# Kernel tuning notes

Hardware: AMD Instinct MI355X
Metric: run time of the kernel (lower is better)

## Reference

```python
import jax, jax.numpy as jnp
import numpy as np

# Model dims (match init_kwargs)
D_MODEL = 2048
H = 16        # query heads
HKV = 4       # kv heads (GQA)
DS = 32       # semantic head dim (compressed)
DG = 32       # geometric head dim (compressed, RoPE'd)
DV = 64       # value head dim
B, T = 2, 4096
MB = 64       # mem_block
LW = 1024     # local_window
ROPE_BASE = 10000.0
NEG_INF = -1e9


def _rope(x, pos, base):
    # x: [B, h, T, d] with d even; standard rotate-half RoPE
    d = x.shape[-1]
    inv_freq = 1.0 / (base ** (jnp.arange(0, d, 2, dtype=jnp.float32) / d))
    ang = pos.astype(jnp.float32)[:, None] * inv_freq          # [T, d/2]
    cos, sin = jnp.cos(ang), jnp.sin(ang)                      # [T, d/2]
    x1, x2 = jnp.split(x, 2, axis=-1)
    return jnp.concatenate([x1 * cos - x2 * sin,
                            x2 * cos + x1 * sin], axis=-1)


def setup_inputs() -> dict:
    key = jax.random.key(0)
    ks = jax.random.split(key, 8)
    w = lambda k, sh: jax.random.normal(k, sh, jnp.float32) * 0.02
    return {
        "x": jax.random.normal(ks[0], (B, T, D_MODEL), jnp.float32),
        "Wq_sem": w(ks[1], (D_MODEL, H * DS)),
        "Wk_sem": w(ks[2], (D_MODEL, HKV * DS)),
        "Wq_geo": w(ks[3], (D_MODEL, H * DG)),
        "Wk_geo": w(ks[4], (D_MODEL, HKV * DG)),
        "Wv": w(ks[5], (D_MODEL, HKV * DV)),
        "Wo": w(ks[6], (H * DV, D_MODEL)),
        "logit_scale": jnp.zeros((H,), jnp.float32),
    }


def reference(x, Wq_sem, Wk_sem, Wq_geo, Wk_geo, Wv, Wo, logit_scale):
    Bq, Tq = x.shape[0], x.shape[1]
    split = lambda y, h, d: y.reshape(Bq, Tq, h, d).transpose(0, 2, 1, 3)
    # Decoupled projections
    q_sem = split(x @ Wq_sem, H, DS)      # [B,H,T,DS]
    k_sem = split(x @ Wk_sem, HKV, DS)    # [B,HKV,T,DS]
    q_geo = split(x @ Wq_geo, H, DG)
    k_geo = split(x @ Wk_geo, HKV, DG)
    v = split(x @ Wv, HKV, DV)            # [B,HKV,T,DV]
    pos = jnp.arange(Tq)
    # RoPE only on the geometric path
    q_geo = _rope(q_geo, pos, ROPE_BASE)
    k_geo = _rope(k_geo, pos, ROPE_BASE)
    # Memory-block summarization: mean-pool remote KV into one token per block
    remote = Tq - LW
    nblk = remote // MB
    pool = lambda a: jnp.concatenate(
        [a[:, :, :remote].reshape(Bq, HKV, nblk, MB, a.shape[-1]).mean(axis=3),
         a[:, :, remote:]], axis=2)
    k_sem2, k_geo2, v2 = pool(k_sem), pool(k_geo), pool(v)  # [B,HKV,K,*], K=nblk+LW
    k_pos = jnp.concatenate([jnp.arange(nblk) * MB + (MB - 1),
                             jnp.arange(remote, Tq)])        # [K]
    # GQA head-group broadcast
    rep = lambda a: jnp.repeat(a, H // HKV, axis=1)
    k_sem2, k_geo2, v2 = rep(k_sem2), rep(k_geo2), rep(v2)   # [B,H,K,*]
    # Decoupled scores: semantic + geometric, each with its own scale
    scores = (jnp.einsum('bhqd,bhkd->bhqk', q_sem, k_sem2) * (1.0 / jnp.sqrt(float(DS)))
              + jnp.einsum('bhqd,bhkd->bhqk', q_geo, k_geo2) * (1.0 / jnp.sqrt(float(DG))))
    # Learned per-head temperature
    scores = scores * jnp.exp(logit_scale)[None, :, None, None]
    # Causal mask over summarized key positions
    mask = k_pos[None, :] <= pos[:, None]                    # [T,K]
    scores = jnp.where(mask[None, None], scores, NEG_INF)
    probs = jax.nn.softmax(scores, axis=-1)
    out = jnp.einsum('bhqk,bhkd->bhqd', probs, v2)           # [B,H,T,DV]
    out = out.transpose(0, 2, 1, 3).reshape(Bq, Tq, H * DV)
    return out @ Wo                                          # [B,T,D_MODEL]
```

## Files before the change

### kernel.cpp

```cpp
#include <hip/hip_runtime.h>
#include <math.h>

#define B_  2
#define T_  4096
#define DM  2048
#define H_  16
#define HKV 4
#define DV_ 64
#define MB_ 64
#define LW_ 1024
#define REMOTE 3072
#define NBLK 48
#define KTOT 1072
#define NTILES 17

typedef __bf16 bf16x8 __attribute__((ext_vector_type(8)));
typedef float  f32x4  __attribute__((ext_vector_type(4)));

__device__ __forceinline__ float bf2f(unsigned short u) {
    unsigned int x = ((unsigned int)u) << 16;
    return __builtin_bit_cast(float, x);
}
__device__ __forceinline__ unsigned short f2bf(float f) {
    unsigned int x = __builtin_bit_cast(unsigned int, f);
    x = x + 0x7fffu + ((x >> 16) & 1u);
    return (unsigned short)(x >> 16);
}

__device__ __forceinline__ void gload16(const unsigned short* gsrc,
                                        unsigned short* ldst) {
    __builtin_amdgcn_global_load_lds(
        (const __attribute__((address_space(1))) void*)gsrc,
        (__attribute__((address_space(3))) void*)ldst,
        16, 0, 0);
}

__global__ void cvt_f32_to_bf16(const float* __restrict__ src,
                                unsigned short* __restrict__ dst, int n) {
    int i = (blockIdx.x * blockDim.x + threadIdx.x) * 4;
    if (i >= n) return;
    float4 v = *(const float4*)(src + i);
    ushort4 o;
    o.x = f2bf(v.x); o.y = f2bf(v.y); o.z = f2bf(v.z); o.w = f2bf(v.w);
    *(ushort4*)(dst + i) = o;
}

__global__ void transpose_cvt(const float* __restrict__ src,
                              unsigned short* __restrict__ dst, int R, int C) {
    __shared__ float tile[32][33];
    int ct = blockIdx.x, rt = blockIdx.y;
    int tx = threadIdx.x, ty = threadIdx.y;
    #pragma unroll
    for (int i = ty; i < 32; i += 8)
        tile[i][tx] = src[(size_t)(rt * 32 + i) * C + ct * 32 + tx];
    __syncthreads();
    #pragma unroll
    for (int i = ty; i < 32; i += 8)
        dst[(size_t)(ct * 32 + i) * R + rt * 32 + tx] = f2bf(tile[tx][i]);
}

template<int MODE>
__global__ __launch_bounds__(512, 2) void gemm8p(
    const unsigned short* __restrict__ A,
    const unsigned short* __restrict__ BT,
    float* __restrict__ outF,
    unsigned short* __restrict__ qcat,
    unsigned short* __restrict__ kp,
    unsigned short* __restrict__ vt,
    int M, int N, int K, int nbx)
{
    extern __shared__ __align__(16) unsigned short lds[];

    const int tid = threadIdx.x;
    const int lane = tid & 63, w = tid >> 6;
    const int wm = w >> 2, wn = w & 3;
    const int l15 = lane & 15, lg = lane >> 4;

    const int cpx = gridDim.x >> 3;
    const int swz = (blockIdx.x & 7) * cpx + (blockIdx.x >> 3);
    const int bx = swz % nbx, by = swz / nbx;
    const int row0 = by * 256, col0 = bx * 256;

    const unsigned short* Ag = A  + (size_t)row0 * K;
    const unsigned short* Bg = BT + (size_t)col0 * K;

    const int sr0 = w * 16 + (lane >> 2);
    const int sr1 = sr0 + 128;
    const int sc0 = ((lane & 3) ^ ((sr0 >> 1) & 3)) << 3;

    const int rdsw = (lg ^ ((l15 >> 1) & 3)) << 3;
    const int aoff = (wm * 128 + l15) * 32 + rdsw;
    const int boff = (wn * 64 + l15) * 32 + rdsw;

    const int NT = K >> 5;
    f32x4 acc[8][4] = {};

    auto stageA = [&](int slot, int kk) {
        unsigned short* sa = lds + slot * 16384;
        gload16(Ag + (size_t)sr0 * K + kk + sc0, sa + w * 512);
        gload16(Ag + (size_t)sr1 * K + kk + sc0, sa + 4096 + w * 512);
    };
    auto stageB = [&](int slot, int kk) {
        unsigned short* sb = lds + slot * 16384 + 8192;
        gload16(Bg + (size_t)sr0 * K + kk + sc0, sb + w * 512);
        gload16(Bg + (size_t)sr1 * K + kk + sc0, sb + 4096 + w * 512);
    };

    stageA(0, 0);  stageB(0, 0);
    stageA(1, 32); stageB(1, 32);
    stageA(2, 64); stageB(2, 64);
    asm volatile("s_waitcnt vmcnt(8)" ::: "memory");

    for (int t = 0; t < NT; ++t) {
        __builtin_amdgcn_s_barrier();
        const unsigned short* As_ = lds + (t & 3) * 16384;
        const unsigned short* Bs_ = As_ + 8192;
        const int wslot = (t + 3) & 3;
        const int kk3 = (t + 3) << 5;
        const bool st = (t + 3) < NT;

        if (st) stageA(wslot, kk3);
        bf16x8 bfr[4], af[4];
        #pragma unroll
        for (int nf = 0; nf < 4; nf++)
            bfr[nf] = __builtin_bit_cast(bf16x8, *(const uint4*)&Bs_[boff + nf * 512]);
        #pragma unroll
        for (int mf = 0; mf < 4; mf++)
            af[mf] = __builtin_bit_cast(bf16x8, *(const uint4*)&As_[aoff + mf * 512]);
        __builtin_amdgcn_s_setprio(1);
        #pragma unroll
        for (int mf = 0; mf < 4; mf++)
            #pragma unroll
            for (int nf = 0; nf < 4; nf++)
                acc[mf][nf] = __builtin_amdgcn_mfma_f32_16x16x32_bf16(
                                  af[mf], bfr[nf], acc[mf][nf], 0, 0, 0);
        __builtin_amdgcn_s_setprio(0);

        if (st) stageB(wslot, kk3);
        bf16x8 af2[4];
        #pragma unroll
        for (int mf = 0; mf < 4; mf++)
            af2[mf] = __builtin_bit_cast(bf16x8, *(const uint4*)&As_[aoff + (mf + 4) * 512]);
        __builtin_amdgcn_s_setprio(1);
        #pragma unroll
        for (int mf = 0; mf < 4; mf++)
            #pragma unroll
            for (int nf = 0; nf < 4; nf++)
                acc[mf + 4][nf] = __builtin_amdgcn_mfma_f32_16x16x32_bf16(
                                      af2[mf], bfr[nf], acc[mf + 4][nf], 0, 0, 0);
        __builtin_amdgcn_s_setprio(0);

        if (t + 3 < NT)      asm volatile("s_waitcnt vmcnt(8)" ::: "memory");
        else if (t + 2 < NT) asm volatile("s_waitcnt vmcnt(4)" ::: "memory");
        else if (t + 1 < NT) asm volatile("s_waitcnt vmcnt(0)" ::: "memory");
    }

    const int rbase = wm * 128;
    if (MODE == 1) {
        #pragma unroll
        for (int mf = 0; mf < 8; mf++)
            #pragma unroll
            for (int nf = 0; nf < 4; nf++)
                #pragma unroll
                for (int r = 0; r < 4; r++) {
                    int row = row0 + rbase + mf * 16 + lg * 4 + r;
                    int col = col0 + wn * 64 + nf * 16 + l15;
                    outF[(size_t)row * N + col] = acc[mf][nf][r];
                }
    } else {
        const int cspan = col0 + wn * 64;
        const int tbase = row0 & 4095;
        const int bq = row0 >> 12;

        if ((cspan >= 512 && cspan < 1024) || (cspan >= 1152 && cspan < 1280)) {
            const float invf = exp2f(-(float)l15 * 0.8304820237218406f);
            #pragma unroll
            for (int mf = 0; mf < 8; mf++) {
                #pragma unroll
                for (int r = 0; r < 4; r++) {
                    float s, c;
                    sincosf((float)(tbase + rbase + mf*16 + lg*4 + r) * invf, &s, &c);
                    float a0 = acc[mf][0][r], a1 = acc[mf][1][r];
                    acc[mf][0][r] = a0 * c - a1 * s;
                    acc[mf][1][r] = a1 * c + a0 * s;
                    float a2 = acc[mf][2][r], a3 = acc[mf][3][r];
                    acc[mf][2][r] = a2 * c - a3 * s;
                    acc[mf][3][r] = a3 * c + a2 * s;
                }
            }
        }

        if (cspan < 1024) {
            #pragma unroll
            for (int nf = 0; nf < 4; nf++) {
                int col = cspan + nf * 16 + l15;
                int h = (col < 512) ? (col >> 5) : ((col - 512) >> 5);
                int d = (col < 512) ? (col & 31) : (32 + (col & 31));
                unsigned short* qb =
                    qcat + (((size_t)(bq * 16 + h)) * 4096 + tbase) * 64 + d;
                #pragma unroll
                for (int mf = 0; mf < 8; mf++)
                    #pragma unroll
                    for (int r = 0; r < 4; r++)
                        qb[(size_t)(rbase + mf*16 + lg*4 + r) * 64] =
                            f2bf(acc[mf][nf][r]);
            }
        } else if (tbase >= REMOTE) {
            #pragma unroll
            for (int nf = 0; nf < 4; nf++) {
                int col = cspan + nf * 16 + l15;
                #pragma unroll
                for (int mf = 0; mf < 8; mf++)
                    #pragma unroll
                    for (int r = 0; r < 4; r++) {
                        int key = tbase + rbase + mf*16 + lg*4 + r - 3024;
                        unsigned short hv = f2bf(acc[mf][nf][r]);
                        if (col < 1280) {
                            int g, dk;
                            if (col < 1152) { g = (col - 1024) >> 5; dk = col & 31; }
                            else            { g = (col - 1152) >> 5; dk = 32 + (col & 31); }
                            kp[(((size_t)(bq*4 + g)) * KTOT + key) * 64 + dk] = hv;
                        } else {
                            int g = (col - 1280) >> 6, dv = col & 63;
                            vt[(((size_t)(bq*4 + g)) * 64 + dv) * KTOT + key] = hv;
                        }
                    }
            }
        } else {
            #pragma unroll
            for (int half = 0; half < 2; half++) {
                #pragma unroll
                for (int nf = 0; nf < 4; nf++) {
                    float ps = 0.f;
                    #pragma unroll
                    for (int mf = half * 4; mf < half * 4 + 4; mf++)
                        #pragma unroll
                        for (int r = 0; r < 4; r++) ps += acc[mf][nf][r];
                    ps += __shfl_xor(ps, 16);
                    ps += __shfl_xor(ps, 32);
                    if (lane < 16) {
                        int col = cspan + nf * 16 + l15;
                        int key = ((tbase + rbase) >> 6) + half;
                        unsigned short hv = f2bf(ps * (1.f / 64.f));
                        if (col < 1280) {
                            int g, dk;
                            if (col < 1152) { g = (col - 1024) >> 5; dk = col & 31; }
                            else            { g = (col - 1152) >> 5; dk = 32 + (col & 31); }
                            kp[(((size_t)(bq*4 + g)) * KTOT + key) * 64 + dk] = hv;
                        } else {
                            int g = (col - 1280) >> 6, dv = col & 63;
                            vt[(((size_t)(bq*4 + g)) * 64 + dv) * KTOT + key] = hv;
                        }
                    }
                }
            }
        }
    }
}

__global__ __launch_bounds__(256) void attn_fwd(
    const unsigned short* __restrict__ qcat,
    const unsigned short* __restrict__ kp,
    const unsigned short* __restrict__ vt,
    const float* __restrict__ ls,
    unsigned short* __restrict__ attn_out)
{
    __shared__ unsigned short Pl[4][32][72];

    const int tid = threadIdx.x;
    const int lane = tid & 63, w = tid >> 6;
    const int l15 = lane & 15, lg = lane >> 4;

    const int wid = blockIdx.x * 4 + w;
    const int hb = wid & 31;
    const int iu = wid >> 5;
    int i;
    if (iu < 32)       i = 127 - iu;
    else if (iu == 32) i = 0;
    else if (iu == 33) i = 1;
    else               i = iu - 32;
    const int h = hb & 15, b = hb >> 4, g = h >> 2;
    const int q0 = i * 32;

    int ktmax;
    if (q0 < 64) ktmax = NTILES;
    else {
        int lastkey = q0 + 31 - 3024;
        ktmax = (lastkey < NBLK) ? 1 : (lastkey / 64 + 1);
    }

    const float sc = __expf(ls[h]) * 0.17677669529663687f;

    bf16x8 aq[2][2];
    const unsigned short* qbase = qcat + (((size_t)(b * 16 + h)) * T_ + q0) * 64;
    #pragma unroll
    for (int rf = 0; rf < 2; rf++)
        #pragma unroll
        for (int kh = 0; kh < 2; kh++)
            aq[rf][kh] = __builtin_bit_cast(bf16x8,
                *(const uint4*)(qbase + (size_t)(rf*16 + l15)*64 + kh*32 + lg*8));

    float m[2][4], lrun[2][4];
    #pragma unroll
    for (int rf = 0; rf < 2; rf++)
        #pragma unroll
        for (int r = 0; r < 4; r++) { m[rf][r] = -1e9f; lrun[rf][r] = 0.f; }
    f32x4 oacc[2][4] = {};

    const unsigned short* kbase = kp + ((size_t)(b * 4 + g)) * KTOT * 64;
    const unsigned short* vbase = vt + ((size_t)(b * 4 + g)) * 64 * KTOT;

    for (int kt = 0; kt < ktmax; kt++) {
        const int kb = kt * 64;

        bf16x8 bk[4][2];
        #pragma unroll
        for (int nf = 0; nf < 4; nf++) {
            int krow = kb + nf*16 + l15;
            int krc = krow < KTOT ? krow : KTOT - 1;
            #pragma unroll
            for (int kh = 0; kh < 2; kh++)
                bk[nf][kh] = __builtin_bit_cast(bf16x8,
                    *(const uint4*)(kbase + (size_t)krc * 64 + kh*32 + lg*8));
        }

        f32x4 s[2][4] = {};
        #pragma unroll
        for (int rf = 0; rf < 2; rf++)
            #pragma unroll
            for (int nf = 0; nf < 4; nf++)
                #pragma unroll
                for (int kh = 0; kh < 2; kh++)
                    s[rf][nf] = __builtin_amdgcn_mfma_f32_16x16x32_bf16(
                                    aq[rf][kh], bk[nf][kh], s[rf][nf], 0, 0, 0);

        bf16x8 bv[4][2];
        #pragma unroll
        for (int nfv = 0; nfv < 4; nfv++)
            #pragma unroll
            for (int kh = 0; kh < 2; kh++) {
                int kc = kb + kh*32 + lg*8;
                int kcc = (kc + 8 <= KTOT) ? kc : KTOT - 8;
                bv[nfv][kh] = __builtin_bit_cast(bf16x8,
                    *(const uint4*)(vbase + (size_t)(nfv*16 + l15) * KTOT + kcc));
            }

        #pragma unroll
        for (int rf = 0; rf < 2; rf++) {
            #pragma unroll
            for (int r = 0; r < 4; r++) {
                const int qpos = q0 + rf*16 + lg*4 + r;
                float vals[4];
                float tmax = -INFINITY;
                #pragma unroll
                for (int nf = 0; nf < 4; nf++) {
                    int key = kb + nf*16 + l15;
                    float v = s[rf][nf][r] * sc;
                    int kpos = (key < NBLK) ? key * 64 + 63 : 3024 + key;
                    v = (key < KTOT) ? ((kpos <= qpos) ? v : -1e9f) : -INFINITY;
                    vals[nf] = v;
                    tmax = fmaxf(tmax, v);
                }
                #pragma unroll
                for (int d = 1; d < 16; d <<= 1)
                    tmax = fmaxf(tmax, __shfl_xor(tmax, d));
                float mn = fmaxf(m[rf][r], tmax);
                float scl = __expf(m[rf][r] - mn);
                m[rf][r] = mn;
                float rs = 0.f;
                #pragma unroll
                for (int nf = 0; nf < 4; nf++) {
                    unsigned short pb = f2bf(__expf(vals[nf] - mn));
                    rs += bf2f(pb);
                    Pl[w][rf*16 + lg*4 + r][nf*16 + l15] = pb;
                }
                #pragma unroll
                for (int d = 1; d < 16; d <<= 1)
                    rs += __shfl_xor(rs, d);
                lrun[rf][r] = lrun[rf][r] * scl + rs;
                #pragma unroll
                for (int nfv = 0; nfv < 4; nfv++)
                    oacc[rf][nfv][r] *= scl;
            }
        }

        #pragma unroll
        for (int rf = 0; rf < 2; rf++) {
            bf16x8 pa[2];
            #pragma unroll
            for (int kh = 0; kh < 2; kh++)
                pa[kh] = __builtin_bit_cast(bf16x8,
                    *(const uint4*)&Pl[w][rf*16 + l15][kh*32 + lg*8]);
            #pragma unroll
            for (int nfv = 0; nfv < 4; nfv++)
                #pragma unroll
                for (int kh = 0; kh < 2; kh++)
                    oacc[rf][nfv] = __builtin_amdgcn_mfma_f32_16x16x32_bf16(
                                        pa[kh], bv[nfv][kh], oacc[rf][nfv], 0, 0, 0);
        }
    }

    #pragma unroll
    for (int rf = 0; rf < 2; rf++) {
        #pragma unroll
        for (int r = 0; r < 4; r++) {
            float inv = 1.f / lrun[rf][r];
            int q = q0 + rf*16 + lg*4 + r;
            size_t obase = ((size_t)(b * T_ + q)) * 1024 + h * 64;
            #pragma unroll
            for (int nfv = 0; nfv < 4; nfv++)
                attn_out[obase + nfv*16 + l15] = f2bf(oacc[rf][nfv][r] * inv);
        }
    }
}

extern "C" void kernel_launch(void* const* d_in, const int* in_sizes, int n_in,
                              void* d_out, int out_size, void* d_ws, size_t ws_size,
                              hipStream_t stream) {
    const float* x      = (const float*)d_in[0];
    const float* Wq_sem = (const float*)d_in[1];
    const float* Wk_sem = (const float*)d_in[2];
    const float* Wq_geo = (const float*)d_in[3];
    const float* Wk_geo = (const float*)d_in[4];
    const float* Wv     = (const float*)d_in[5];
    const float* Wo     = (const float*)d_in[6];
    const float* ls     = (const float*)d_in[7];

    char* w = (char*)d_ws;
    auto alloc = [&](size_t bytes) {
        char* p = w;
        w += (bytes + 255) & ~(size_t)255;
        return p;
    };
    unsigned short* xb    = (unsigned short*)alloc((size_t)8192 * 2048 * 2);
    unsigned short* WcatT = (unsigned short*)alloc((size_t)1536 * 2048 * 2);
    unsigned short* WoT   = (unsigned short*)alloc((size_t)2048 * 1024 * 2);
    unsigned short* qcat  = (unsigned short*)alloc((size_t)2 * 16 * 4096 * 64 * 2);
    unsigned short* kp    = (unsigned short*)alloc((size_t)2 * 4 * 1072 * 64 * 2);
    unsigned short* vt    = (unsigned short*)alloc((size_t)2 * 4 * 1072 * 64 * 2);
    unsigned short* aout  = (unsigned short*)alloc((size_t)8192 * 1024 * 2);

    hipFuncSetAttribute(reinterpret_cast<const void*>(&gemm8p<0>),
                        hipFuncAttributeMaxDynamicSharedMemorySize, 131072);
    hipFuncSetAttribute(reinterpret_cast<const void*>(&gemm8p<1>),
                        hipFuncAttributeMaxDynamicSharedMemorySize, 131072);

    cvt_f32_to_bf16<<<16384, 256, 0, stream>>>(x, xb, 8192 * 2048);

    dim3 tb(32, 8);
    transpose_cvt<<<dim3(16, 64), tb, 0, stream>>>(Wq_sem, WcatT + (size_t)0    * 2048, 2048, 512);
    transpose_cvt<<<dim3(16, 64), tb, 0, stream>>>(Wq_geo, WcatT + (size_t)512  * 2048, 2048, 512);
    transpose_cvt<<<dim3( 4, 64), tb, 0, stream>>>(Wk_sem, WcatT + (size_t)1024 * 2048, 2048, 128);
    transpose_cvt<<<dim3( 4, 64), tb, 0, stream>>>(Wk_geo, WcatT + (size_t)1152 * 2048, 2048, 128);
    transpose_cvt<<<dim3( 8, 64), tb, 0, stream>>>(Wv,     WcatT + (size_t)1280 * 2048, 2048, 256);
    transpose_cvt<<<dim3(64, 32), tb, 0, stream>>>(Wo, WoT, 1024, 2048);

    gemm8p<0><<<192, 512, 131072, stream>>>(
        xb, WcatT, nullptr, qcat, kp, vt, 8192, 1536, 2048, 6);

    attn_fwd<<<dim3(1024), 256, 0, stream>>>(qcat, kp, vt, ls, aout);

    gemm8p<1><<<256, 512, 131072, stream>>>(
        aout, WoT, (float*)d_out, nullptr, nullptr, nullptr, 8192, 2048, 1024, 8);
}
```

Measured before the change: 214.4 us.

## Restructure GEMM main loop into K=64 ping-pong with fine-grained staged loads

Rewrites the bf16 GEMM mainloop so that each LDS stage covers a K=64 slice (two MFMA k-steps), double-buffered as A0/B0 and A1/B1. Each stage is split into four sub-phases over quadrants of the 8x4 accumulator tile, and the global-to-LDS loads for the next tile are interleaved between them under barriers, using a new 8-way XOR swizzle. The aim is better overlap of global loads with MFMA work and fewer LDS reads per MFMA, at the cost of many more barriers per iteration.

```diff
diff --git a/kernel.cpp b/kernel.cpp
--- a/kernel.cpp
+++ b/kernel.cpp
@@ -60,7 +60,7 @@
 }
 
 template<int MODE>
-__global__ __launch_bounds__(512, 2) void gemm8p(
+__global__ __launch_bounds__(512, 2) void gemm8f(
     const unsigned short* __restrict__ A,
     const unsigned short* __restrict__ BT,
     float* __restrict__ outF,
@@ -84,76 +84,209 @@
     const unsigned short* Ag = A  + (size_t)row0 * K;
     const unsigned short* Bg = BT + (size_t)col0 * K;
 
-    const int sr0 = w * 16 + (lane >> 2);
-    const int sr1 = sr0 + 128;
-    const int sc0 = ((lane & 3) ^ ((sr0 >> 1) & 3)) << 3;
-
-    const int rdsw = (lg ^ ((l15 >> 1) & 3)) << 3;
-    const int aoff = (wm * 128 + l15) * 32 + rdsw;
-    const int boff = (wn * 64 + l15) * 32 + rdsw;
-
-    const int NT = K >> 5;
+    unsigned short* const A0 = lds;
+    unsigned short* const B0 = lds + 16384;
+    unsigned short* const A1 = lds + 32768;
+    unsigned short* const B1 = lds + 49152;
+
+    const int srow  = w * 8 + (lane >> 3);
+    const int scol8 = ((lane & 7) ^ ((lane >> 3) & 7)) * 8;
+
+    const int l7 = lane & 7;
+    const int p0 = ((lg) ^ l7) * 8;
+    const int p1 = ((4 + lg) ^ l7) * 8;
+    const int arow = (wm * 128 + l15) * 64;
+    const int brow = (wn * 64 + l15) * 64;
+
+    const int NT = K >> 6;
+    const int NI = NT >> 1;
     f32x4 acc[8][4] = {};
 
-    auto stageA = [&](int slot, int kk) {
-        unsigned short* sa = lds + slot * 16384;
-        gload16(Ag + (size_t)sr0 * K + kk + sc0, sa + w * 512);
-        gload16(Ag + (size_t)sr1 * K + kk + sc0, sa + 4096 + w * 512);
+    auto stgA = [&](unsigned short* Ab, int half, int tt) {
+        unsigned short* hb = Ab + half * 8192;
+        const unsigned short* src =
+            Ag + (size_t)(half * 128 + srow) * K + tt * 64 + scol8;
+        gload16(src, hb + w * 512);
+        gload16(src + (size_t)64 * K, hb + 4096 + w * 512);
     };
-    auto stageB = [&](int slot, int kk) {
-        unsigned short* sb = lds + slot * 16384 + 8192;
-        gload16(Bg + (size_t)sr0 * K + kk + sc0, sb + w * 512);
-        gload16(Bg + (size_t)sr1 * K + kk + sc0, sb + 4096 + w * 512);
+    auto stgB = [&](unsigned short* Bb, int half, int tt) {
+        unsigned short* hb = Bb + half * 8192;
+        const unsigned short* src =
+            Bg + (size_t)(half * 128 + srow) * K + tt * 64 + scol8;
+        gload16(src, hb + w * 512);
+        gload16(src + (size_t)64 * K, hb + 4096 + w * 512);
     };
 
-    stageA(0, 0);  stageB(0, 0);
-    stageA(1, 32); stageB(1, 32);
-    stageA(2, 64); stageB(2, 64);
-    asm volatile("s_waitcnt vmcnt(8)" ::: "memory");
-
-    for (int t = 0; t < NT; ++t) {
-        __builtin_amdgcn_s_barrier();
-        const unsigned short* As_ = lds + (t & 3) * 16384;
-        const unsigned short* Bs_ = As_ + 8192;
-        const int wslot = (t + 3) & 3;
-        const int kk3 = (t + 3) << 5;
-        const bool st = (t + 3) < NT;
-
-        if (st) stageA(wslot, kk3);
-        bf16x8 bfr[4], af[4];
-        #pragma unroll
-        for (int nf = 0; nf < 4; nf++)
-            bfr[nf] = __builtin_bit_cast(bf16x8, *(const uint4*)&Bs_[boff + nf * 512]);
-        #pragma unroll
-        for (int mf = 0; mf < 4; mf++)
-            af[mf] = __builtin_bit_cast(bf16x8, *(const uint4*)&As_[aoff + mf * 512]);
-        __builtin_amdgcn_s_setprio(1);
-        #pragma unroll
-        for (int mf = 0; mf < 4; mf++)
-            #pragma unroll
-            for (int nf = 0; nf < 4; nf++)
-                acc[mf][nf] = __builtin_amdgcn_mfma_f32_16x16x32_bf16(
-                                  af[mf], bfr[nf], acc[mf][nf], 0, 0, 0);
-        __builtin_amdgcn_s_setprio(0);
-
-        if (st) stageB(wslot, kk3);
-        bf16x8 af2[4];
-        #pragma unroll
-        for (int mf = 0; mf < 4; mf++)
-            af2[mf] = __builtin_bit_cast(bf16x8, *(const uint4*)&As_[aoff + (mf + 4) * 512]);
-        __builtin_amdgcn_s_setprio(1);
-        #pragma unroll
-        for (int mf = 0; mf < 4; mf++)
-            #pragma unroll
-            for (int nf = 0; nf < 4; nf++)
-                acc[mf + 4][nf] = __builtin_amdgcn_mfma_f32_16x16x32_bf16(
-                                      af2[mf], bfr[nf], acc[mf + 4][nf], 0, 0, 0);
-        __builtin_amdgcn_s_setprio(0);
-
-        if (t + 3 < NT)      asm volatile("s_waitcnt vmcnt(8)" ::: "memory");
-        else if (t + 2 < NT) asm volatile("s_waitcnt vmcnt(4)" ::: "memory");
-        else if (t + 1 < NT) asm volatile("s_waitcnt vmcnt(0)" ::: "memory");
+    #define LDF(base, off) __builtin_bit_cast(bf16x8, *(const uint4*)&(base)[off])
+
+    stgB(B0, 0, 0); stgB(B0, 1, 0);
+    stgA(A0, 0, 0); stgA(A0, 1, 0);
+    stgB(B1, 0, 1); stgB(B1, 1, 1);
+    asm volatile("s_waitcnt vmcnt(4)" ::: "memory");
+    __builtin_amdgcn_s_barrier();
+
+    for (int i = 0; i < NI; ++i) {
+        const int t0 = 2 * i;
+        const bool st2 = (t0 + 2) < NT;
+        bf16x8 af[4][2], b01[2][2], b23[2][2];
+
+        #pragma unroll
+        for (int mf = 0; mf < 4; mf++) {
+            af[mf][0] = LDF(A0, arow + mf * 1024 + p0);
+            af[mf][1] = LDF(A0, arow + mf * 1024 + p1);
+        }
+        #pragma unroll
+        for (int nf = 0; nf < 2; nf++) {
+            b01[nf][0] = LDF(B0, brow + nf * 1024 + p0);
+            b01[nf][1] = LDF(B0, brow + nf * 1024 + p1);
+        }
+        stgA(A1, 0, t0 + 1);
+        __builtin_amdgcn_s_barrier();
+        __builtin_amdgcn_s_setprio(1);
+        #pragma unroll
+        for (int mf = 0; mf < 4; mf++)
+            #pragma unroll
+            for (int nf = 0; nf < 2; nf++)
+                #pragma unroll
+                for (int ks = 0; ks < 2; ks++)
+                    acc[mf][nf] = __builtin_amdgcn_mfma_f32_16x16x32_bf16(
+                        af[mf][ks], b01[nf][ks], acc[mf][nf], 0, 0, 0);
+        __builtin_amdgcn_s_setprio(0);
+        __builtin_amdgcn_s_barrier();
+
+        #pragma unroll
+        for (int nf = 0; nf < 2; nf++) {
+            b23[nf][0] = LDF(B0, brow + (nf + 2) * 1024 + p0);
+            b23[nf][1] = LDF(B0, brow + (nf + 2) * 1024 + p1);
+        }
+        stgA(A1, 1, t0 + 1);
+        __builtin_amdgcn_s_barrier();
+        __builtin_amdgcn_s_setprio(1);
+        #pragma unroll
+        for (int mf = 0; mf < 4; mf++)
+            #pragma unroll
+            for (int nf = 0; nf < 2; nf++)
+                #pragma unroll
+                for (int ks = 0; ks < 2; ks++)
+                    acc[mf][nf + 2] = __builtin_amdgcn_mfma_f32_16x16x32_bf16(
+                        af[mf][ks], b23[nf][ks], acc[mf][nf + 2], 0, 0, 0);
+        __builtin_amdgcn_s_setprio(0);
+        __builtin_amdgcn_s_barrier();
+
+        #pragma unroll
+        for (int mf = 0; mf < 4; mf++) {
+            af[mf][0] = LDF(A0, arow + (mf + 4) * 1024 + p0);
+            af[mf][1] = LDF(A0, arow + (mf + 4) * 1024 + p1);
+        }
+        if (st2) stgB(B0, 0, t0 + 2);
+        __builtin_amdgcn_s_barrier();
+        __builtin_amdgcn_s_setprio(1);
+        #pragma unroll
+        for (int mf = 0; mf < 4; mf++)
+            #pragma unroll
+            for (int nf = 0; nf < 2; nf++)
+                #pragma unroll
+                for (int ks = 0; ks < 2; ks++)
+                    acc[mf + 4][nf] = __builtin_amdgcn_mfma_f32_16x16x32_bf16(
+                        af[mf][ks], b01[nf][ks], acc[mf + 4][nf], 0, 0, 0);
+        __builtin_amdgcn_s_setprio(0);
+        __builtin_amdgcn_s_barrier();
+
+        if (st2) stgB(B0, 1, t0 + 2);
+        __builtin_amdgcn_s_barrier();
+        __builtin_amdgcn_s_setprio(1);
+        #pragma unroll
+        for (int mf = 0; mf < 4; mf++)
+            #pragma unroll
+            for (int nf = 0; nf < 2; nf++)
+                #pragma unroll
+                for (int ks = 0; ks < 2; ks++)
+                    acc[mf + 4][nf + 2] = __builtin_amdgcn_mfma_f32_16x16x32_bf16(
+                        af[mf][ks], b23[nf][ks], acc[mf + 4][nf + 2], 0, 0, 0);
+        __builtin_amdgcn_s_setprio(0);
+        if (st2) asm volatile("s_waitcnt vmcnt(4)" ::: "memory");
+        else     asm volatile("s_waitcnt vmcnt(0)" ::: "memory");
+        __builtin_amdgcn_s_barrier();
+
+        #pragma unroll
+        for (int mf = 0; mf < 4; mf++) {
+            af[mf][0] = LDF(A1, arow + mf * 1024 + p0);
+            af[mf][1] = LDF(A1, arow + mf * 1024 + p1);
+        }
+        #pragma unroll
+        for (int nf = 0; nf < 2; nf++) {
+            b01[nf][0] = LDF(B1, brow + nf * 1024 + p0);
+            b01[nf][1] = LDF(B1, brow + nf * 1024 + p1);
+        }
+        if (st2) stgA(A0, 0, t0 + 2);
+        __builtin_amdgcn_s_barrier();
+        __builtin_amdgcn_s_setprio(1);
+        #pragma unroll
+        for (int mf = 0; mf < 4; mf++)
+            #pragma unroll
+            for (int nf = 0; nf < 2; nf++)
+                #pragma unroll
+                for (int ks = 0; ks < 2; ks++)
+                    acc[mf][nf] = __builtin_amdgcn_mfma_f32_16x16x32_bf16(
+                        af[mf][ks], b01[nf][ks], acc[mf][nf], 0, 0, 0);
+        __builtin_amdgcn_s_setprio(0);
+        __builtin_amdgcn_s_barrier();
+
+        #pragma unroll
+        for (int nf = 0; nf < 2; nf++) {
+            b23[nf][0] = LDF(B1, brow + (nf + 2) * 1024 + p0);
+            b23[nf][1] = LDF(B1, brow + (nf + 2) * 1024 + p1);
+        }
+        if (st2) stgA(A0, 1, t0 + 2);
+        __builtin_amdgcn_s_barrier();
+        __builtin_amdgcn_s_setprio(1);
+        #pragma unroll
+        for (int mf = 0; mf < 4; mf++)
+            #pragma unroll
+            for (int nf = 0; nf < 2; nf++)
+                #pragma unroll
+                for (int ks = 0; ks < 2; ks++)
+                    acc[mf][nf + 2] = __builtin_amdgcn_mfma_f32_16x16x32_bf16(
+                        af[mf][ks], b23[nf][ks], acc[mf][nf + 2], 0, 0, 0);
+        __builtin_amdgcn_s_setprio(0);
+        __builtin_amdgcn_s_barrier();
+
+        #pragma unroll
+        for (int mf = 0; mf < 4; mf++) {
+            af[mf][0] = LDF(A1, arow + (mf + 4) * 1024 + p0);
+            af[mf][1] = LDF(A1, arow + (mf + 4) * 1024 + p1);
+        }
+        if (st2) stgB(B1, 0, t0 + 3);
+        __builtin_amdgcn_s_barrier();
+        __builtin_amdgcn_s_setprio(1);
+        #pragma unroll
+        for (int mf = 0; mf < 4; mf++)
+            #pragma unroll
+            for (int nf = 0; nf < 2; nf++)
+                #pragma unroll
+                for (int ks = 0; ks < 2; ks++)
+                    acc[mf + 4][nf] = __builtin_amdgcn_mfma_f32_16x16x32_bf16(
+                        af[mf][ks], b01[nf][ks], acc[mf + 4][nf], 0, 0, 0);
+        __builtin_amdgcn_s_setprio(0);
+        __builtin_amdgcn_s_barrier();
+
+        if (st2) stgB(B1, 1, t0 + 3);
+        __builtin_amdgcn_s_barrier();
+        __builtin_amdgcn_s_setprio(1);
+        #pragma unroll
+        for (int mf = 0; mf < 4; mf++)
+            #pragma unroll
+            for (int nf = 0; nf < 2; nf++)
+                #pragma unroll
+                for (int ks = 0; ks < 2; ks++)
+                    acc[mf + 4][nf + 2] = __builtin_amdgcn_mfma_f32_16x16x32_bf16(
+                        af[mf][ks], b23[nf][ks], acc[mf + 4][nf + 2], 0, 0, 0);
+        __builtin_amdgcn_s_setprio(0);
+        if (st2) asm volatile("s_waitcnt vmcnt(4)" ::: "memory");
+        else     asm volatile("s_waitcnt vmcnt(0)" ::: "memory");
+        __builtin_amdgcn_s_barrier();
     }
+    #undef LDF
 
     const int rbase = wm * 128;
     if (MODE == 1) {
@@ -440,9 +573,9 @@
     unsigned short* vt    = (unsigned short*)alloc((size_t)2 * 4 * 1072 * 64 * 2);
     unsigned short* aout  = (unsigned short*)alloc((size_t)8192 * 1024 * 2);
 
-    hipFuncSetAttribute(reinterpret_cast<const void*>(&gemm8p<0>),
+    hipFuncSetAttribute(reinterpret_cast<const void*>(&gemm8f<0>),
                         hipFuncAttributeMaxDynamicSharedMemorySize, 131072);
-    hipFuncSetAttribute(reinterpret_cast<const void*>(&gemm8p<1>),
+    hipFuncSetAttribute(reinterpret_cast<const void*>(&gemm8f<1>),
                         hipFuncAttributeMaxDynamicSharedMemorySize, 131072);
 
     cvt_f32_to_bf16<<<16384, 256, 0, stream>>>(x, xb, 8192 * 2048);
@@ -455,11 +588,11 @@
     transpose_cvt<<<dim3( 8, 64), tb, 0, stream>>>(Wv,     WcatT + (size_t)1280 * 2048, 2048, 256);
     transpose_cvt<<<dim3(64, 32), tb, 0, stream>>>(Wo, WoT, 1024, 2048);
 
-    gemm8p<0><<<192, 512, 131072, stream>>>(
+    gemm8f<0><<<192, 512, 131072, stream>>>(
         xb, WcatT, nullptr, qcat, kp, vt, 8192, 1536, 2048, 6);
 
     attn_fwd<<<dim3(1024), 256, 0, stream>>>(qcat, kp, vt, ls, aout);
 
-    gemm8p<1><<<256, 512, 131072, stream>>>(
+    gemm8f<1><<<256, 512, 131072, stream>>>(
         aout, WoT, (float*)d_out, nullptr, nullptr, nullptr, 8192, 2048, 1024, 8);
 }
```

After: 214.7 us. Within noise of the previous version (+0.2%).
